# Kernel tuning notes

Hardware: AMD Instinct MI355X
Metric: run time of the kernel (lower is better)

Reference implementation:

```python
import jax, jax.numpy as jnp
import numpy as np

B, H, W, C_IN, C_OUT, KH, KW = 32, 56, 56, 128, 256, 3, 3


def setup_inputs() -> dict:
    key = jax.random.key(0)
    k1, k2, k3 = jax.random.split(key, 3)
    x = jax.random.normal(k1, (B, H, W, C_IN), dtype=jnp.float32)
    w = jax.random.normal(k2, (KH, KW, C_IN, C_OUT), dtype=jnp.float32) * 0.05
    b = jax.random.normal(k3, (C_OUT,), dtype=jnp.float32) * 0.05
    return {"x": x, "w": w, "b": b}


def reference(x, w, b):
    # SAME-padded, stride-1 2D conv (math identical to the im2col loop in the
    # original, collapsed into a single conv/GEMM) plus bias.
    out = jax.lax.conv_general_dilated(
        x, w,
        window_strides=(1, 1),
        padding="SAME",
        dimension_numbers=("NHWC", "HWIO", "NHWC"),
    )
    return out + b
```

## Files before the change

kernel.cpp:

```cpp
#include <hip/hip_runtime.h>

#define B_ 32
#define CI 128
#define CO 256
#define K_DIM 1152
#define M_DIM 100352
#define BM 128
#define BN 256
#define BK 32
#define KTILES 36
#define HPAD 58
#define XB_OFF 589824

typedef float          floatx4  __attribute__((ext_vector_type(4)));
typedef unsigned short ushortx8 __attribute__((ext_vector_type(8)));
typedef __bf16         bf16x8   __attribute__((ext_vector_type(8)));

typedef __attribute__((address_space(1))) void gas_void;
typedef __attribute__((address_space(3))) void las_void;
#define GLD16(g, l) __builtin_amdgcn_global_load_lds( \
    (gas_void*)(uintptr_t)(g), (las_void*)(l), 16, 0, 0)

__device__ __forceinline__ unsigned short bf16_rne(float f) {
    unsigned u = __builtin_bit_cast(unsigned, f);
    u += 0x7FFFu + ((u >> 16) & 1u);
    return (unsigned short)(u >> 16);
}

__global__ void wt_transpose_kernel(const float* __restrict__ w,
                                    unsigned short* __restrict__ wt) {
    __shared__ unsigned short tile[64][65];
    const int kt = blockIdx.x * 64, nt = blockIdx.y * 64;
    #pragma unroll
    for (int i = 0; i < 16; ++i) {
        int idx = i * 256 + threadIdx.x;
        int kl = idx >> 6, nl = idx & 63;
        tile[kl][nl] = bf16_rne(w[(size_t)(kt + kl) * CO + nt + nl]);
    }
    __syncthreads();
    #pragma unroll
    for (int i = 0; i < 16; ++i) {
        int idx = i * 256 + threadIdx.x;
        int nl = idx >> 6, kl = idx & 63;
        wt[(size_t)(nt + nl) * K_DIM + kt + kl] = tile[kl][nl];
    }
}

__global__ void xpad_kernel(const float* __restrict__ x,
                            unsigned short* __restrict__ xb) {
    const int t   = blockIdx.x * 256 + threadIdx.x;
    const int pix = t >> 4;
    const int cc  = (t & 15) << 3;
    const int b   = pix / (HPAD * HPAD);
    const int rem = pix % (HPAD * HPAD);
    const int hp  = rem / HPAD, wp = rem % HPAD;
    ushortx8 g = {0, 0, 0, 0, 0, 0, 0, 0};
    if (hp >= 1 && hp <= 56 && wp >= 1 && wp <= 56) {
        const float* s = x + ((size_t)((b * 56 + hp - 1) * 56 + (wp - 1))) * CI + cc;
        floatx4 f0 = ((const floatx4*)s)[0];
        floatx4 f1 = ((const floatx4*)s)[1];
        #pragma unroll
        for (int e = 0; e < 4; ++e) { g[e] = bf16_rne(f0[e]); g[e + 4] = bf16_rne(f1[e]); }
    }
    *(ushortx8*)(xb + (size_t)pix * CI + cc) = g;
}

__global__ __launch_bounds__(512, 4)
void conv_gemm_kernel(const unsigned short* __restrict__ xb,
                      const unsigned short* __restrict__ wt,
                      const float* __restrict__ bias,
                      float* __restrict__ out) {
    __shared__ unsigned short As[2][BM * BK];
    __shared__ unsigned short Bs[2][BN * BK];

    const int tid  = threadIdx.x;
    const int by   = blockIdx.x;
    const int wid  = tid >> 6;
    const int lane = tid & 63;
    const int lrow = lane & 15;
    const int quad = lane >> 4;
    const int wm   = (wid & 1) * 64;
    const int wn   = (wid >> 1) * 64;

    const int rseg = lane >> 2;
    const int cglb = ((lane & 3) - (rseg >> 1)) & 3;

    const int ar = wid * 16 + rseg;
    const int m0 = by * BM + ar;
    const int b0 = m0 / 3136, r0 = m0 % 3136;
    const unsigned short* ag0 = xb + ((size_t)((b0 * HPAD + r0 / 56) * HPAD + r0 % 56)) * CI + cglb * 8;

    const int nr0 = wid * 32 + rseg;
    const unsigned short* bg0 = wt + (size_t)nr0 * K_DIM + cglb * 8;
    const unsigned short* bg1 = bg0 + (size_t)16 * K_DIM;

    const int ldsA  = (wid * 16) * BK;
    const int ldsB0 = (wid * 32) * BK;
    const int ldsB1 = ldsB0 + 16 * BK;

    const int swz = ((quad + (lrow >> 1)) & 3) * 8;
    int a_idx[4], b_idx[4];
    #pragma unroll
    for (int i = 0; i < 4; ++i) {
        a_idx[i] = (wm + i * 16 + lrow) * BK + swz;
        b_idx[i] = (wn + i * 16 + lrow) * BK + swz;
    }

    floatx4 acc[4][4] = {};

    auto stage = [&](int kb, int buf) {
        const int p    = kb >> 2;
        const int c0   = (kb & 3) << 5;
        const int aoff = (p / 3 * HPAD + p % 3) * CI + c0;
        const int boff = kb * BK;
        GLD16(ag0 + aoff, &As[buf][ldsA]);
        GLD16(bg0 + boff, &Bs[buf][ldsB0]);
        GLD16(bg1 + boff, &Bs[buf][ldsB1]);
    };

    auto compute = [&](int buf) {
        ushortx8 arv[4], brv[4];
        #pragma unroll
        for (int mi = 0; mi < 4; ++mi) arv[mi] = *(const ushortx8*)&As[buf][a_idx[mi]];
        #pragma unroll
        for (int ni = 0; ni < 4; ++ni) brv[ni] = *(const ushortx8*)&Bs[buf][b_idx[ni]];
        #pragma unroll
        for (int mi = 0; mi < 4; ++mi)
            #pragma unroll
            for (int ni = 0; ni < 4; ++ni)
                acc[mi][ni] = __builtin_amdgcn_mfma_f32_16x16x32_bf16(
                    __builtin_bit_cast(bf16x8, arv[mi]),
                    __builtin_bit_cast(bf16x8, brv[ni]),
                    acc[mi][ni], 0, 0, 0);
    };

    stage(0, 0);
    __syncthreads();
    int cur = 0;
    #pragma unroll 1
    for (int kb = 0; kb < KTILES - 1; ++kb) {
        stage(kb + 1, cur ^ 1);
        compute(cur);
        __syncthreads();
        cur ^= 1;
    }
    compute(cur);

    float bv[4];
    #pragma unroll
    for (int ni = 0; ni < 4; ++ni)
        bv[ni] = bias[wn + ni * 16 + lrow];

    #pragma unroll
    for (int mi = 0; mi < 4; ++mi) {
        #pragma unroll
        for (int r = 0; r < 4; ++r) {
            const int row = by * BM + wm + mi * 16 + quad * 4 + r;
            float* o = out + (size_t)row * CO + wn + lrow;
            #pragma unroll
            for (int ni = 0; ni < 4; ++ni)
                o[ni * 16] = acc[mi][ni][r] + bv[ni];
        }
    }
}

extern "C" void kernel_launch(void* const* d_in, const int* in_sizes, int n_in,
                              void* d_out, int out_size, void* d_ws, size_t ws_size,
                              hipStream_t stream) {
    (void)in_sizes; (void)n_in; (void)out_size; (void)ws_size;
    const float* x    = (const float*)d_in[0];
    const float* w    = (const float*)d_in[1];
    const float* bias = (const float*)d_in[2];
    float* out = (float*)d_out;

    unsigned short* wt = (unsigned short*)d_ws;
    unsigned short* xb = (unsigned short*)((char*)d_ws + XB_OFF);

    wt_transpose_kernel<<<dim3(K_DIM / 64, CO / 64), dim3(256), 0, stream>>>(w, wt);
    xpad_kernel<<<dim3((B_ * HPAD * HPAD * 16) / 256), dim3(256), 0, stream>>>(x, xb);
    conv_gemm_kernel<<<dim3(M_DIM / BM), dim3(512), 0, stream>>>(xb, wt, bias, out);
}
```

Measured before the change: 212.7 us.

## Triple-buffer GEMM main loop with one barrier per tile and fuse prepass kernels

Moves the conv GEMM from double to triple LDS buffering. Each tile now waits on the in-flight global-to-LDS loads with explicit vmcnt and takes a single barrier, so loads are issued two tiles ahead instead of one. The MFMA block runs at raised wave priority via s_setprio. The weight transpose and input pad/convert kernels are merged into one launch to save a kernel boundary. The cost is 50% more LDS per block, which may lower occupancy under launch_bounds(512,4), and the hand-written waitcnt depends on exactly three loads per stage.

```diff
diff --git a/kernel.cpp b/kernel.cpp
--- a/kernel.cpp
+++ b/kernel.cpp
@@ -9,8 +9,11 @@
 #define BN 256
 #define BK 32
 #define KTILES 36
+#define NBUF 3
 #define HPAD 58
 #define XB_OFF 589824
+#define WTBLK 72
+#define XPBLK 6728
 
 typedef float          floatx4  __attribute__((ext_vector_type(4)));
 typedef unsigned short ushortx8 __attribute__((ext_vector_type(8)));
@@ -27,42 +30,43 @@
     return (unsigned short)(u >> 16);
 }
 
-__global__ void wt_transpose_kernel(const float* __restrict__ w,
-                                    unsigned short* __restrict__ wt) {
+__global__ void prepass_kernel(const float* __restrict__ x,
+                               const float* __restrict__ w,
+                               unsigned short* __restrict__ xb,
+                               unsigned short* __restrict__ wt) {
     __shared__ unsigned short tile[64][65];
-    const int kt = blockIdx.x * 64, nt = blockIdx.y * 64;
-    #pragma unroll
-    for (int i = 0; i < 16; ++i) {
-        int idx = i * 256 + threadIdx.x;
-        int kl = idx >> 6, nl = idx & 63;
-        tile[kl][nl] = bf16_rne(w[(size_t)(kt + kl) * CO + nt + nl]);
+    if (blockIdx.x < WTBLK) {
+        const int kt = (blockIdx.x % 18) * 64, nt = (blockIdx.x / 18) * 64;
+        #pragma unroll
+        for (int i = 0; i < 16; ++i) {
+            int idx = i * 256 + threadIdx.x;
+            int kl = idx >> 6, nl = idx & 63;
+            tile[kl][nl] = bf16_rne(w[(size_t)(kt + kl) * CO + nt + nl]);
+        }
+        __syncthreads();
+        #pragma unroll
+        for (int i = 0; i < 16; ++i) {
+            int idx = i * 256 + threadIdx.x;
+            int nl = idx >> 6, kl = idx & 63;
+            wt[(size_t)(nt + nl) * K_DIM + kt + kl] = tile[kl][nl];
+        }
+    } else {
+        const int t   = (blockIdx.x - WTBLK) * 256 + threadIdx.x;
+        const int pix = t >> 4;
+        const int cc  = (t & 15) << 3;
+        const int b   = pix / (HPAD * HPAD);
+        const int rem = pix % (HPAD * HPAD);
+        const int hp  = rem / HPAD, wp = rem % HPAD;
+        ushortx8 g = {0, 0, 0, 0, 0, 0, 0, 0};
+        if (hp >= 1 && hp <= 56 && wp >= 1 && wp <= 56) {
+            const float* s = x + ((size_t)((b * 56 + hp - 1) * 56 + (wp - 1))) * CI + cc;
+            floatx4 f0 = ((const floatx4*)s)[0];
+            floatx4 f1 = ((const floatx4*)s)[1];
+            #pragma unroll
+            for (int e = 0; e < 4; ++e) { g[e] = bf16_rne(f0[e]); g[e + 4] = bf16_rne(f1[e]); }
+        }
+        *(ushortx8*)(xb + (size_t)pix * CI + cc) = g;
     }
-    __syncthreads();
-    #pragma unroll
-    for (int i = 0; i < 16; ++i) {
-        int idx = i * 256 + threadIdx.x;
-        int nl = idx >> 6, kl = idx & 63;
-        wt[(size_t)(nt + nl) * K_DIM + kt + kl] = tile[kl][nl];
-    }
-}
-
-__global__ void xpad_kernel(const float* __restrict__ x,
-                            unsigned short* __restrict__ xb) {
-    const int t   = blockIdx.x * 256 + threadIdx.x;
-    const int pix = t >> 4;
-    const int cc  = (t & 15) << 3;
-    const int b   = pix / (HPAD * HPAD);
-    const int rem = pix % (HPAD * HPAD);
-    const int hp  = rem / HPAD, wp = rem % HPAD;
-    ushortx8 g = {0, 0, 0, 0, 0, 0, 0, 0};
-    if (hp >= 1 && hp <= 56 && wp >= 1 && wp <= 56) {
-        const float* s = x + ((size_t)((b * 56 + hp - 1) * 56 + (wp - 1))) * CI + cc;
-        floatx4 f0 = ((const floatx4*)s)[0];
-        floatx4 f1 = ((const floatx4*)s)[1];
-        #pragma unroll
-        for (int e = 0; e < 4; ++e) { g[e] = bf16_rne(f0[e]); g[e + 4] = bf16_rne(f1[e]); }
-    }
-    *(ushortx8*)(xb + (size_t)pix * CI + cc) = g;
 }
 
 __global__ __launch_bounds__(512, 4)
@@ -70,8 +74,8 @@
                       const unsigned short* __restrict__ wt,
                       const float* __restrict__ bias,
                       float* __restrict__ out) {
-    __shared__ unsigned short As[2][BM * BK];
-    __shared__ unsigned short Bs[2][BN * BK];
+    __shared__ unsigned short As[NBUF][BM * BK];
+    __shared__ unsigned short Bs[NBUF][BN * BK];
 
     const int tid  = threadIdx.x;
     const int by   = blockIdx.x;
@@ -124,6 +128,7 @@
         for (int mi = 0; mi < 4; ++mi) arv[mi] = *(const ushortx8*)&As[buf][a_idx[mi]];
         #pragma unroll
         for (int ni = 0; ni < 4; ++ni) brv[ni] = *(const ushortx8*)&Bs[buf][b_idx[ni]];
+        __builtin_amdgcn_s_setprio(1);
         #pragma unroll
         for (int mi = 0; mi < 4; ++mi)
             #pragma unroll
@@ -132,19 +137,29 @@
                     __builtin_bit_cast(bf16x8, arv[mi]),
                     __builtin_bit_cast(bf16x8, brv[ni]),
                     acc[mi][ni], 0, 0, 0);
+        __builtin_amdgcn_s_setprio(0);
     };
 
     stage(0, 0);
-    __syncthreads();
-    int cur = 0;
+    stage(1, 1);
+
+#define ITER(T, BC, BS)                                                  \
+    do {                                                                 \
+        if ((T) < KTILES - 1) asm volatile("s_waitcnt vmcnt(3)" ::: "memory"); \
+        else                  asm volatile("s_waitcnt vmcnt(0)" ::: "memory"); \
+        __builtin_amdgcn_s_barrier();                                    \
+        asm volatile("" ::: "memory");                                   \
+        if ((T) + 2 < KTILES) stage((T) + 2, (BS));                      \
+        compute((BC));                                                   \
+    } while (0)
+
     #pragma unroll 1
-    for (int kb = 0; kb < KTILES - 1; ++kb) {
-        stage(kb + 1, cur ^ 1);
-        compute(cur);
-        __syncthreads();
-        cur ^= 1;
+    for (int tt = 0; tt < KTILES; tt += 3) {
+        ITER(tt + 0, 0, 2);
+        ITER(tt + 1, 1, 0);
+        ITER(tt + 2, 2, 1);
     }
-    compute(cur);
+#undef ITER
 
     float bv[4];
     #pragma unroll
@@ -176,7 +191,6 @@
     unsigned short* wt = (unsigned short*)d_ws;
     unsigned short* xb = (unsigned short*)((char*)d_ws + XB_OFF);
 
-    wt_transpose_kernel<<<dim3(K_DIM / 64, CO / 64), dim3(256), 0, stream>>>(w, wt);
-    xpad_kernel<<<dim3((B_ * HPAD * HPAD * 16) / 256), dim3(256), 0, stream>>>(x, xb);
+    prepass_kernel<<<dim3(WTBLK + XPBLK), dim3(256), 0, stream>>>(x, w, xb, wt);
     conv_gemm_kernel<<<dim3(M_DIM / BM), dim3(512), 0, stream>>>(xb, wt, bias, out);
 }
```

New measurement: 212.0 us. Within noise of the previous version (-0.4%).
